# Performance work log

Hardware: AMD Instinct MI355X
Metric: run time of the kernel (lower is better)

The kernel has to match this reference:

```python
import jax, jax.numpy as jnp
import numpy as np

B, C, H, W = 64, 512, 32, 32
R = 32  # reduction_channels = max(512 // 16, 8)


def setup_inputs() -> dict:
    key = jax.random.key(0)
    ks = jax.random.split(key, 10)
    s = 0.05
    return {
        "x": jax.random.normal(ks[0], (B, C, H, W), jnp.float32),
        "w_fc1": jax.random.normal(ks[1], (R, C), jnp.float32) * s,
        "b_fc1": jax.random.normal(ks[2], (R,), jnp.float32) * s,
        "w_fc2": jax.random.normal(ks[3], (C, R), jnp.float32) * s,
        "b_fc2": jax.random.normal(ks[4], (C,), jnp.float32) * s,
        "w_eig": jax.random.normal(ks[5], (R, C), jnp.float32) * s,
        "b_eig": jax.random.normal(ks[6], (R,), jnp.float32) * s,
        "w_sp": jax.random.normal(ks[7], (C,), jnp.float32) * s,
        "b_sp": jax.random.normal(ks[8], (1,), jnp.float32) * s,
        # random init vector for power iteration (torch.randn in the module)
        "v0": jax.random.normal(ks[9], (B, R, 1), jnp.float32),
    }


def reference(x, w_fc1, b_fc1, w_fc2, b_fc2, w_eig, b_eig, w_sp, b_sp, v0):
    b, c, h, w = x.shape
    hw = h * w

    # ---- channel attention (SE): global avg pool -> fc1 -> relu -> fc2 -> sigmoid
    pooled = jnp.mean(x, axis=(2, 3))                     # [B, C]
    ca = jax.nn.relu(jnp.einsum("bc,rc->br", pooled, w_fc1) + b_fc1)
    ca = jax.nn.sigmoid(jnp.einsum("br,cr->bc", ca, w_fc2) + b_fc2)
    channel_att = ca[:, :, None, None]                    # [B, C, 1, 1]

    # ---- eigen attention branch
    feat = jnp.einsum("bchw,rc->brhw", x, w_eig) + b_eig[None, :, None, None]
    feat = feat.reshape(b, R, hw)                         # [B, R, HW]
    feat_c = feat - jnp.mean(feat, axis=2, keepdims=True)
    cov = jnp.einsum("brn,bsn->brs", feat_c, feat_c) / (hw - 1)
    cov = cov + 1e-5 * jnp.eye(R, dtype=x.dtype)

    v = v0 / jnp.linalg.norm(v0, axis=1, keepdims=True)
    for _ in range(5):  # 5-step power iteration
        v = jnp.einsum("brs,bsi->bri", cov, v)
        v = v / (jnp.linalg.norm(v, axis=1, keepdims=True) + 1e-10)

    att = jnp.einsum("bri,brn->bn", v, feat_c).reshape(b, 1, h, w)
    amin = jnp.min(att, axis=(2, 3), keepdims=True)
    att = att - amin
    amax = jnp.max(att, axis=(2, 3), keepdims=True)
    eigen_att = jax.nn.sigmoid(att / (amax + 1e-10))      # [B, 1, H, W]

    # ---- spatial attention: 1x1 conv C->1 -> sigmoid
    spatial_att = jax.nn.sigmoid(
        jnp.einsum("bchw,c->bhw", x, w_sp)[:, None] + b_sp[0]
    )                                                      # [B, 1, H, W]

    att_all = eigen_att * spatial_att
    return x * channel_att * att_all + x
```

## Files before the change

kernel.cpp:

```cpp
#include <hip/hip_runtime.h>
#include <hip/hip_bf16.h>

#define B_ 64
#define C_ 512
#define HW_ 1024
#define R_ 32
#define NPXG 16

typedef __attribute__((ext_vector_type(8))) short bf16x8;
typedef __attribute__((ext_vector_type(4))) float f32x4;

union U8 { uint4 q; bf16x8 v; unsigned short s[8]; };

__device__ __forceinline__ unsigned short f2bf(float f) {
    __hip_bfloat16 h = __float2bfloat16(f);
    union { __hip_bfloat16 b; unsigned short u; } c; c.b = h; return c.u;
}

__device__ __forceinline__ float dpp_fold16(float s) {
    int y;
    y = __builtin_amdgcn_update_dpp(0, __float_as_int(s), 0xB1, 0xF, 0xF, true);
    s += __int_as_float(y);
    y = __builtin_amdgcn_update_dpp(0, __float_as_int(s), 0x4E, 0xF, 0xF, true);
    s += __int_as_float(y);
    y = __builtin_amdgcn_update_dpp(0, __float_as_int(s), 0x141, 0xF, 0xF, true);
    s += __int_as_float(y);
    y = __builtin_amdgcn_update_dpp(0, __float_as_int(s), 0x140, 0xF, 0xF, true);
    s += __int_as_float(y);
    return s;
}

__global__ void k_prep(const float* __restrict__ w_eig,
                       const float* __restrict__ w_sp,
                       uint4* __restrict__ wfrag) {
    int idx   = blockIdx.x * 256 + threadIdx.x;
    int lane  = idx & 63;
    int kstep = (idx >> 6) & 15;
    int slot  = idx >> 10;
    int m = lane & 15, g = lane >> 4;
    int cbase = kstep * 32 + 8 * g;

    U8 u;
    if (slot < 2) {
        int r = slot * 16 + m;
#pragma unroll
        for (int i = 0; i < 8; ++i) u.s[i] = f2bf(w_eig[r * C_ + cbase + i]);
    } else {
#pragma unroll
        for (int i = 0; i < 8; ++i)
            u.s[i] = (m == 0) ? f2bf(w_sp[cbase + i]) : (unsigned short)0;
    }
    wfrag[idx] = u.q;
}

__global__ __launch_bounds__(256, 4) void k_proj(
    const float* __restrict__ x, const uint4* __restrict__ wfrag,
    __hip_bfloat16* __restrict__ featp, float* __restrict__ spp,
    float* __restrict__ pooledp)
{
    const int t    = threadIdx.x;
    const int lane = t & 63;
    const int wv   = t >> 6;
    const int blk  = blockIdx.x;
    const int b    = blk >> 4;
    const int pxg  = blk & 15;
    const int px0  = pxg * 64 + wv * 16;
    const int g    = lane >> 4;
    const int col  = lane & 15;
    const int px   = px0 + col;

    __shared__ float plds[C_][5];

    f32x4 acc0 = {0.f, 0.f, 0.f, 0.f};
    f32x4 acc1 = {0.f, 0.f, 0.f, 0.f};
    f32x4 acc2 = {0.f, 0.f, 0.f, 0.f};

    const float* xb = x + (size_t)b * C_ * HW_ + px;
    const uint4* wf = wfrag + lane;

    for (int ks = 0; ks < 16; ++ks) {
        const int c8 = ks * 32 + 8 * g;
        const float* xc = xb + (size_t)c8 * HW_;

        float x0 = xc[0 * HW_], x1 = xc[1 * HW_], x2 = xc[2 * HW_],
              x3 = xc[3 * HW_], x4 = xc[4 * HW_], x5 = xc[5 * HW_],
              x6 = xc[6 * HW_], x7 = xc[7 * HW_];

        U8 a0, a1, a2, bu;
        a0.q = wf[(0 * 16 + ks) * 64];
        a1.q = wf[(1 * 16 + ks) * 64];
        a2.q = wf[(2 * 16 + ks) * 64];
        bu.s[0] = f2bf(x0); bu.s[1] = f2bf(x1);
        bu.s[2] = f2bf(x2); bu.s[3] = f2bf(x3);
        bu.s[4] = f2bf(x4); bu.s[5] = f2bf(x5);
        bu.s[6] = f2bf(x6); bu.s[7] = f2bf(x7);

        acc0 = __builtin_amdgcn_mfma_f32_16x16x32_bf16(a0.v, bu.v, acc0, 0, 0, 0);
        acc1 = __builtin_amdgcn_mfma_f32_16x16x32_bf16(a1.v, bu.v, acc1, 0, 0, 0);
        acc2 = __builtin_amdgcn_mfma_f32_16x16x32_bf16(a2.v, bu.v, acc2, 0, 0, 0);

        float s0 = dpp_fold16(x0), s1 = dpp_fold16(x1);
        float s2 = dpp_fold16(x2), s3 = dpp_fold16(x3);
        float s4 = dpp_fold16(x4), s5 = dpp_fold16(x5);
        float s6 = dpp_fold16(x6), s7 = dpp_fold16(x7);
        if (col == 0) {
            plds[c8 + 0][wv] = s0; plds[c8 + 1][wv] = s1;
            plds[c8 + 2][wv] = s2; plds[c8 + 3][wv] = s3;
            plds[c8 + 4][wv] = s4; plds[c8 + 5][wv] = s5;
            plds[c8 + 6][wv] = s6; plds[c8 + 7][wv] = s7;
        }
    }

    if (lane < 16) spp[(size_t)b * HW_ + px0 + lane] = acc2.x;

    __hip_bfloat16* fb = featp + ((size_t)b * HW_ + px) * R_;
    ushort4 p0, p1;
    p0.x = f2bf(acc0.x); p0.y = f2bf(acc0.y);
    p0.z = f2bf(acc0.z); p0.w = f2bf(acc0.w);
    p1.x = f2bf(acc1.x); p1.y = f2bf(acc1.y);
    p1.z = f2bf(acc1.z); p1.w = f2bf(acc1.w);
    *(ushort4*)(fb + 4 * g)      = p0;
    *(ushort4*)(fb + 16 + 4 * g) = p1;

    __syncthreads();
    for (int c = t; c < C_; c += 256) {
        float s = plds[c][0] + plds[c][1] + plds[c][2] + plds[c][3];
        pooledp[((size_t)pxg * B_ + b) * C_ + c] = s;
    }
}

__device__ __forceinline__ float dpp_fold8(float s) {
    int y;
    y = __builtin_amdgcn_update_dpp(0, __float_as_int(s), 0xB1, 0xF, 0xF, true);
    s += __int_as_float(y);
    y = __builtin_amdgcn_update_dpp(0, __float_as_int(s), 0x4E, 0xF, 0xF, true);
    s += __int_as_float(y);
    y = __builtin_amdgcn_update_dpp(0, __float_as_int(s), 0x141, 0xF, 0xF, true);
    s += __int_as_float(y);
    return s;
}

__global__ __launch_bounds__(1024) void k_eigen(
    const __hip_bfloat16* __restrict__ featp, const float* __restrict__ spp,
    const float* __restrict__ pooledp,
    const float* __restrict__ w_eig, const float* __restrict__ w_fc1,
    const float* __restrict__ b_fc1, const float* __restrict__ w_fc2,
    const float* __restrict__ b_fc2, const float* __restrict__ b_sp,
    const float* __restrict__ v0,
    float* __restrict__ ca_out, float* __restrict__ att_out)
{
    const int b    = blockIdx.x;
    const int t    = threadIdx.x;
    const int lane = t & 63;
    const int wave = t >> 6;

    __shared__ float pooledm[C_];
    __shared__ float meanv[R_], t1[R_], vv[R_], wred[R_];
    __shared__ float plds2[R_ / 2][128][2];
    __shared__ float redmn[16], redmx[16], scal[2];

    if (t < C_) {
        float s = 0.f;
#pragma unroll
        for (int pg = 0; pg < NPXG; ++pg)
            s += pooledp[((size_t)pg * B_ + b) * C_ + t];
        pooledm[t] = s * (1.f / 1024.f);
    }
    __syncthreads();

    if (t < 512) {
        const int r = t >> 4, k = t & 15;
        float pm = 0.f, pf = 0.f;
        for (int c = k; c < C_; c += 16) {
            float p = pooledm[c];
            pm = fmaf(w_eig[r * C_ + c], p, pm);
            pf = fmaf(w_fc1[r * C_ + c], p, pf);
        }
#pragma unroll
        for (int m = 8; m > 0; m >>= 1) {
            pm += __shfl_xor(pm, m, 64);
            pf += __shfl_xor(pf, m, 64);
        }
        if (k == 0) { meanv[r] = pm; t1[r] = fmaxf(pf + b_fc1[r], 0.f); }
    }
    __syncthreads();

    if (t < C_) {
        float s = b_fc2[t];
        const float4* w4 = (const float4*)(w_fc2 + (size_t)t * R_);
#pragma unroll
        for (int k = 0; k < 8; ++k) {
            float4 w = w4[k];
            s = fmaf(w.x, t1[4 * k + 0], s);
            s = fmaf(w.y, t1[4 * k + 1], s);
            s = fmaf(w.z, t1[4 * k + 2], s);
            s = fmaf(w.w, t1[4 * k + 3], s);
        }
        ca_out[b * C_ + t] = 1.f / (1.f + expf(-s));
    }

    float col[R_];
    {
        union { __hip_bfloat16 h[R_]; uint4 qv[4]; } u;
        const uint4* src = (const uint4*)(featp + ((size_t)b * HW_ + t) * R_);
#pragma unroll
        for (int k = 0; k < 4; ++k) u.qv[k] = src[k];
#pragma unroll
        for (int r = 0; r < R_; ++r)
            col[r] = __bfloat162float(u.h[r]) - meanv[r];
    }

    if (t < 64) {
        float vl = (t < R_) ? v0[b * R_ + t] : 0.f;
        float sq = vl * vl;
#pragma unroll
        for (int m = 32; m > 0; m >>= 1) sq += __shfl_xor(sq, m, 64);
        if (t < R_) vv[t] = vl / sqrtf(sq);
    }
    __syncthreads();

    for (int it = 0; it < 5; ++it) {
        float uacc = 0.f;
#pragma unroll
        for (int r = 0; r < R_; ++r) uacc = fmaf(col[r], vv[r], uacc);
        uacc *= (1.f / 1023.f);

#pragma unroll
        for (int gg = 0; gg < R_ / 2; ++gg) {
            float s0 = dpp_fold8(col[2 * gg + 0] * uacc);
            float s1 = dpp_fold8(col[2 * gg + 1] * uacc);
            if ((t & 7) == 0) {
                plds2[gg][t >> 3][0] = s0;
                plds2[gg][t >> 3][1] = s1;
            }
        }
        __syncthreads();

        {
            const int r = t >> 5, i = t & 31;
            const int gg = r >> 1, e = r & 1;
            float s = plds2[gg][i][e] + plds2[gg][i + 32][e] +
                      plds2[gg][i + 64][e] + plds2[gg][i + 96][e];
#pragma unroll
            for (int m = 16; m > 0; m >>= 1) s += __shfl_xor(s, m, 64);
            if (i == 0) wred[r] = s;
        }
        __syncthreads();

        if (t < 64) {
            float w = (t < R_) ? wred[t] + 1e-5f * vv[t] : 0.f;
            float sq = w * w;
#pragma unroll
            for (int m = 32; m > 0; m >>= 1) sq += __shfl_xor(sq, m, 64);
            if (t < R_) vv[t] = w / (sqrtf(sq) + 1e-10f);
        }
        __syncthreads();
    }

    float a = 0.f;
#pragma unroll
    for (int r = 0; r < R_; ++r) a = fmaf(col[r], vv[r], a);

    float mn = a, mx = a;
#pragma unroll
    for (int m = 32; m > 0; m >>= 1) {
        mn = fminf(mn, __shfl_xor(mn, m, 64));
        mx = fmaxf(mx, __shfl_xor(mx, m, 64));
    }
    if (lane == 0) { redmn[wave] = mn; redmx[wave] = mx; }
    __syncthreads();
    if (t == 0) {
        float m1 = redmn[0], m2 = redmx[0];
        for (int w = 1; w < 16; ++w) {
            m1 = fminf(m1, redmn[w]);
            m2 = fmaxf(m2, redmx[w]);
        }
        scal[0] = m1; scal[1] = m2;
    }
    __syncthreads();

    const float amin  = scal[0];
    const float denom = (scal[1] - scal[0]) + 1e-10f;
    float eig = 1.f / (1.f + expf(-((a - amin) / denom)));

    float spsig = 1.f / (1.f + expf(-(b_sp[0] + spp[(size_t)b * HW_ + t])));

    att_out[b * HW_ + t] = eig * spsig;
}

__global__ __launch_bounds__(256) void k_final(
    const float* __restrict__ x, const float* __restrict__ ca,
    const float* __restrict__ att, float* __restrict__ out)
{
    const int t   = threadIdx.x;
    const int blk = blockIdx.x;
    const int b   = blk >> 9;
    const float cav  = ca[blk];
    const size_t base = (size_t)blk * HW_;

    float4 xv = ((const float4*)(x + base))[t];
    float4 av = ((const float4*)(att + (size_t)b * HW_))[t];
    float4 o;
    o.x = fmaf(xv.x * cav, av.x, xv.x);
    o.y = fmaf(xv.y * cav, av.y, xv.y);
    o.z = fmaf(xv.z * cav, av.z, xv.z);
    o.w = fmaf(xv.w * cav, av.w, xv.w);
    ((float4*)(out + base))[t] = o;
}

extern "C" void kernel_launch(void* const* d_in, const int* in_sizes, int n_in,
                              void* d_out, int out_size, void* d_ws, size_t ws_size,
                              hipStream_t stream) {
    const float* x     = (const float*)d_in[0];
    const float* w_fc1 = (const float*)d_in[1];
    const float* b_fc1 = (const float*)d_in[2];
    const float* w_fc2 = (const float*)d_in[3];
    const float* b_fc2 = (const float*)d_in[4];
    const float* w_eig = (const float*)d_in[5];
    const float* w_sp  = (const float*)d_in[7];
    const float* b_sp  = (const float*)d_in[8];
    const float* v0    = (const float*)d_in[9];
    float* out = (float*)d_out;

    char* ws = (char*)d_ws;
    __hip_bfloat16* featp = (__hip_bfloat16*)ws;
    float* spp     = (float*)(ws + 4194304);
    float* pooledp = (float*)(ws + 4456448);
    float* ca      = (float*)(ws + 6553600);
    float* att     = (float*)(ws + 6684672);
    uint4* wfrag   = (uint4*)(ws + 6946816);

    k_prep<<<12, 256, 0, stream>>>(w_eig, w_sp, wfrag);
    k_proj<<<B_ * NPXG, 256, 0, stream>>>(x, wfrag, featp, spp, pooledp);
    k_eigen<<<B_, 1024, 0, stream>>>(featp, spp, pooledp, w_eig, w_fc1, b_fc1,
                                     w_fc2, b_fc2, b_sp, v0, ca, att);
    k_final<<<B_ * C_, 256, 0, stream>>>(x, ca, att, out);
}
```

Before: 94.83 us.

## Split projection K across waves and double pixel groups for more blocks

After: 99.98 us. +5.4%, slower.

```diff
diff --git a/kernel.cpp b/kernel.cpp
--- a/kernel.cpp
+++ b/kernel.cpp
@@ -5,7 +5,7 @@
 #define C_ 512
 #define HW_ 1024
 #define R_ 32
-#define NPXG 16
+#define NPXG 32
 
 typedef __attribute__((ext_vector_type(8))) short bf16x8;
 typedef __attribute__((ext_vector_type(4))) float f32x4;
@@ -53,7 +53,7 @@
     wfrag[idx] = u.q;
 }
 
-__global__ __launch_bounds__(256, 4) void k_proj(
+__global__ __launch_bounds__(256, 8) void k_proj(
     const float* __restrict__ x, const uint4* __restrict__ wfrag,
     __hip_bfloat16* __restrict__ featp, float* __restrict__ spp,
     float* __restrict__ pooledp)
@@ -61,15 +61,18 @@
     const int t    = threadIdx.x;
     const int lane = t & 63;
     const int wv   = t >> 6;
+    const int tile = wv & 1;
+    const int kh   = wv >> 1;
     const int blk  = blockIdx.x;
-    const int b    = blk >> 4;
-    const int pxg  = blk & 15;
-    const int px0  = pxg * 64 + wv * 16;
+    const int b    = blk >> 5;
+    const int pxg  = blk & 31;
+    const int px0  = pxg * 32 + tile * 16;
     const int g    = lane >> 4;
     const int col  = lane & 15;
     const int px   = px0 + col;
 
-    __shared__ float plds[C_][5];
+    __shared__ float plds[C_][3];
+    __shared__ float comb[2][12][64];
 
     f32x4 acc0 = {0.f, 0.f, 0.f, 0.f};
     f32x4 acc1 = {0.f, 0.f, 0.f, 0.f};
@@ -78,8 +81,9 @@
     const float* xb = x + (size_t)b * C_ * HW_ + px;
     const uint4* wf = wfrag + lane;
 
-    for (int ks = 0; ks < 16; ++ks) {
-        const int c8 = ks * 32 + 8 * g;
+    for (int ks = 0; ks < 8; ++ks) {
+        const int kstep = kh * 8 + ks;
+        const int c8 = kstep * 32 + 8 * g;
         const float* xc = xb + (size_t)c8 * HW_;
 
         float x0 = xc[0 * HW_], x1 = xc[1 * HW_], x2 = xc[2 * HW_],
@@ -87,9 +91,9 @@
               x6 = xc[6 * HW_], x7 = xc[7 * HW_];
 
         U8 a0, a1, a2, bu;
-        a0.q = wf[(0 * 16 + ks) * 64];
-        a1.q = wf[(1 * 16 + ks) * 64];
-        a2.q = wf[(2 * 16 + ks) * 64];
+        a0.q = wf[(0 * 16 + kstep) * 64];
+        a1.q = wf[(1 * 16 + kstep) * 64];
+        a2.q = wf[(2 * 16 + kstep) * 64];
         bu.s[0] = f2bf(x0); bu.s[1] = f2bf(x1);
         bu.s[2] = f2bf(x2); bu.s[3] = f2bf(x3);
         bu.s[4] = f2bf(x4); bu.s[5] = f2bf(x5);
@@ -104,28 +108,45 @@
         float s4 = dpp_fold16(x4), s5 = dpp_fold16(x5);
         float s6 = dpp_fold16(x6), s7 = dpp_fold16(x7);
         if (col == 0) {
-            plds[c8 + 0][wv] = s0; plds[c8 + 1][wv] = s1;
-            plds[c8 + 2][wv] = s2; plds[c8 + 3][wv] = s3;
-            plds[c8 + 4][wv] = s4; plds[c8 + 5][wv] = s5;
-            plds[c8 + 6][wv] = s6; plds[c8 + 7][wv] = s7;
-        }
-    }
-
-    if (lane < 16) spp[(size_t)b * HW_ + px0 + lane] = acc2.x;
-
-    __hip_bfloat16* fb = featp + ((size_t)b * HW_ + px) * R_;
-    ushort4 p0, p1;
-    p0.x = f2bf(acc0.x); p0.y = f2bf(acc0.y);
-    p0.z = f2bf(acc0.z); p0.w = f2bf(acc0.w);
-    p1.x = f2bf(acc1.x); p1.y = f2bf(acc1.y);
-    p1.z = f2bf(acc1.z); p1.w = f2bf(acc1.w);
-    *(ushort4*)(fb + 4 * g)      = p0;
-    *(ushort4*)(fb + 16 + 4 * g) = p1;
-
-    __syncthreads();
+            plds[c8 + 0][tile] = s0; plds[c8 + 1][tile] = s1;
+            plds[c8 + 2][tile] = s2; plds[c8 + 3][tile] = s3;
+            plds[c8 + 4][tile] = s4; plds[c8 + 5][tile] = s5;
+            plds[c8 + 6][tile] = s6; plds[c8 + 7][tile] = s7;
+        }
+    }
+    __syncthreads();
+
     for (int c = t; c < C_; c += 256) {
-        float s = plds[c][0] + plds[c][1] + plds[c][2] + plds[c][3];
-        pooledp[((size_t)pxg * B_ + b) * C_ + c] = s;
+        pooledp[((size_t)pxg * B_ + b) * C_ + c] = plds[c][0] + plds[c][1];
+    }
+
+    if (kh == 1) {
+        comb[tile][0][lane] = acc0.x; comb[tile][1][lane] = acc0.y;
+        comb[tile][2][lane] = acc0.z; comb[tile][3][lane] = acc0.w;
+        comb[tile][4][lane] = acc1.x; comb[tile][5][lane] = acc1.y;
+        comb[tile][6][lane] = acc1.z; comb[tile][7][lane] = acc1.w;
+        comb[tile][8][lane] = acc2.x; comb[tile][9][lane] = acc2.y;
+        comb[tile][10][lane] = acc2.z; comb[tile][11][lane] = acc2.w;
+    }
+    __syncthreads();
+    if (kh == 0) {
+        acc0.x += comb[tile][0][lane]; acc0.y += comb[tile][1][lane];
+        acc0.z += comb[tile][2][lane]; acc0.w += comb[tile][3][lane];
+        acc1.x += comb[tile][4][lane]; acc1.y += comb[tile][5][lane];
+        acc1.z += comb[tile][6][lane]; acc1.w += comb[tile][7][lane];
+        acc2.x += comb[tile][8][lane]; acc2.y += comb[tile][9][lane];
+        acc2.z += comb[tile][10][lane]; acc2.w += comb[tile][11][lane];
+
+        if (lane < 16) spp[(size_t)b * HW_ + px0 + lane] = acc2.x;
+
+        __hip_bfloat16* fb = featp + ((size_t)b * HW_ + px) * R_;
+        ushort4 p0, p1;
+        p0.x = f2bf(acc0.x); p0.y = f2bf(acc0.y);
+        p0.z = f2bf(acc0.z); p0.w = f2bf(acc0.w);
+        p1.x = f2bf(acc1.x); p1.y = f2bf(acc1.y);
+        p1.z = f2bf(acc1.z); p1.w = f2bf(acc1.w);
+        *(ushort4*)(fb + 4 * g)      = p0;
+        *(ushort4*)(fb + 16 + 4 * g) = p1;
     }
 }
 
@@ -326,9 +347,9 @@
     __hip_bfloat16* featp = (__hip_bfloat16*)ws;
     float* spp     = (float*)(ws + 4194304);
     float* pooledp = (float*)(ws + 4456448);
-    float* ca      = (float*)(ws + 6553600);
-    float* att     = (float*)(ws + 6684672);
-    uint4* wfrag   = (uint4*)(ws + 6946816);
+    float* ca      = (float*)(ws + 8650752);
+    float* att     = (float*)(ws + 8781824);
+    uint4* wfrag   = (uint4*)(ws + 9043968);
 
     k_prep<<<12, 256, 0, stream>>>(w_eig, w_sp, wfrag);
     k_proj<<<B_ * NPXG, 256, 0, stream>>>(x, wfrag, featp, spp, pooledp);
```
